# Optimization experiments

Measured on AMD Instinct MI355X. Metric: run time of the kernel, lower is better.

## Reference

```python
import jax, jax.numpy as jnp
import numpy as np

N = 500_000      # active sparse sites
C1 = 128         # input channels (c1)
CH = 64          # hidden channels c_ = int(c2 * e)
C2 = 128         # output channels (c2)
B, H, W = 4, 1024, 1024
EPS = 1e-5       # BatchNorm eps


def _build_rulebook(rng):
    """Random unique active sites + 3x3 submanifold neighbor index table.

    nbr[k, i] = row index of the active neighbor of site i at kernel offset k,
    or the sentinel N if that neighbor position is inactive / out of bounds.
    """
    per = N // B
    coords = []
    for b in range(B):
        lin = rng.choice(H * W, size=per, replace=False)
        coords.append(np.stack([np.full(per, b), lin // W, lin % W], axis=1))
    coords = np.concatenate(coords).astype(np.int64)  # [N, 3] = (batch, y, x)
    lut = np.full(B * H * W, N, dtype=np.int64)
    lut[coords[:, 0] * H * W + coords[:, 1] * W + coords[:, 2]] = np.arange(N)
    nbr = np.full((9, N), N, dtype=np.int64)
    k = 0
    for dy in (-1, 0, 1):
        for dx in (-1, 0, 1):
            ny, nx = coords[:, 1] + dy, coords[:, 2] + dx
            valid = (ny >= 0) & (ny < H) & (nx >= 0) & (nx < W)
            lin = coords[:, 0] * H * W + ny * W + nx
            nbr[k, valid] = lut[lin[valid]]
            k += 1
    return nbr


def setup_inputs() -> dict:
    nbr = _build_rulebook(np.random.default_rng(0))
    key = jax.random.key(0)
    ks = jax.random.split(key, 16)
    s = lambda k, shp, sc: (jax.random.normal(k, shp, jnp.float32) * sc)
    inp = {
        "features": jax.random.normal(ks[0], (N, C1), jnp.float32),
        "nbr_idx": jnp.asarray(nbr),
        "W1": s(ks[1], (C1, CH), 0.05),
        "W2": s(ks[2], (9, CH, CH), 0.05),
        "W3": s(ks[3], (CH, C2), 0.05),
        "g1": 1.0 + s(ks[4], (CH,), 0.1),
        "b1": s(ks[5], (CH,), 0.1),
        "m1": s(ks[6], (CH,), 0.1),
        "v1": jax.random.uniform(ks[7], (CH,), jnp.float32) + 0.5,
        "g2": 1.0 + s(ks[8], (CH,), 0.1),
        "b2": s(ks[9], (CH,), 0.1),
        "m2": s(ks[10], (CH,), 0.1),
        "v2": jax.random.uniform(ks[11], (CH,), jnp.float32) + 0.5,
        "g3": 1.0 + s(ks[12], (C2,), 0.1),
        "b3": s(ks[13], (C2,), 0.1),
        "m3": s(ks[14], (C2,), 0.1),
        "v3": jax.random.uniform(ks[15], (C2,), jnp.float32) + 0.5,
    }
    return inp


def _bn(x, g, b, m, v):
    # BatchNorm1d in inference form (running stats)
    return (x - m) * (g * jax.lax.rsqrt(v + EPS)) + b


def reference(features, nbr_idx, W1, W2, W3,
              g1, b1, m1, v1, g2, b2, m2, v2, g3, b3, m3, v3):
    # cv1: 1x1 submanifold conv == dense matmul on features, then BN + SiLU
    h = jax.nn.silu(_bn(features @ W1, g1, b1, m1, v1))  # [N, CH]
    # cv2: 3x3 submanifold conv via rulebook gather-matmul-scatter.
    # Pad one zero row so the sentinel index N gathers zeros (inactive neighbor).
    hp = jnp.concatenate([h, jnp.zeros((1, CH), h.dtype)], axis=0)  # [N+1, CH]
    out = jnp.zeros((features.shape[0], CH), h.dtype)
    for k in range(9):  # fixed kernel-offset loop, not a data-dim loop
        out = out + hp[nbr_idx[k]] @ W2[k]
    out = jax.nn.silu(_bn(out, g2, b2, m2, v2))
    # cv3: 1x1 conv + BN, then residual add (c1 == c2, shortcut) + SiLU
    out = _bn(out @ W3, g3, b3, m3, v3)
    return jax.nn.silu(out + features)
```

## Files before the change

kernel.cpp:

```cpp
#include <hip/hip_runtime.h>

#define DEVINL __device__ __forceinline__

constexpr int N_SITES = 500000;
constexpr int C1 = 128;
constexpr int CH = 64;
constexpr int C2 = 128;
constexpr float BN_EPS = 1e-5f;
constexpr int NT32 = N_SITES / 32;

typedef __attribute__((ext_vector_type(4))) float f32x4;
typedef __attribute__((ext_vector_type(8))) short s16x8;

DEVINL float bf2f(unsigned short s) { return __uint_as_float(((unsigned)s) << 16); }
DEVINL unsigned short f2bf(float f) {
  unsigned u = __float_as_uint(f);
  return (unsigned short)((u + 0x7fffu + ((u >> 16) & 1u)) >> 16);
}
DEVINL float silu_f(float x) { return x / (1.0f + __expf(-x)); }

template<bool F32>
DEVINL float rdf(const void* p, long i) {
  if constexpr (F32) return ((const float*)p)[i];
  else return bf2f(((const unsigned short*)p)[i]);
}

DEVINL bool probe_f32(const void* buf) {
  unsigned w = ((const unsigned*)buf)[threadIdx.x & 63];
  unsigned e = (w >> 7) & 0xFFu;
  bool bf_like = (e >= 90u && e <= 134u) || ((w & 0xFFFFu) == 0u);
  return __popcll(__ballot(bf_like)) < 48;
}
DEVINL bool probe_i64(const int* nbr) {
  int v = nbr[2 * (threadIdx.x & 63) + 1];
  return __popcll(__ballot(v == 0)) == 64;
}
template<bool I64>
DEVINL int rd_idx(const int* nbr, long ofs) {
  if constexpr (I64) return nbr[2 * ofs];
  else return nbr[ofs];
}

DEVINL s16x8 as_s16x8(uint4 v) { union { uint4 u; s16x8 s; } c; c.u = v; return c.s; }

DEVINL s16x8 pack8(float a0, float a1, float a2, float a3,
                   float a4, float a5, float a6, float a7) {
  uint4 r;
  r.x = (unsigned)f2bf(a0) | ((unsigned)f2bf(a1) << 16);
  r.y = (unsigned)f2bf(a2) | ((unsigned)f2bf(a3) << 16);
  r.z = (unsigned)f2bf(a4) | ((unsigned)f2bf(a5) << 16);
  r.w = (unsigned)f2bf(a6) | ((unsigned)f2bf(a7) << 16);
  return as_s16x8(r);
}

DEVINL f32x4 mfma16(s16x8 a, s16x8 b, f32x4 c) {
  return __builtin_amdgcn_mfma_f32_16x16x32_bf16(a, b, c, 0, 0, 0);
}


template<bool F32>
DEVINL void cv1_body(const void* feat, const void* W1,
                     const void* g1, const void* b1, const void* m1, const void* v1,
                     unsigned short* __restrict__ h,
                     unsigned short* lw1, float* lsc, float* ltb,
                     unsigned short* sb )
{
  const int tid = threadIdx.x;
  for (int n = tid; n < CH; n += 256) {
    float s = rdf<F32>(g1, n) * rsqrtf(rdf<F32>(v1, n) + BN_EPS);
    lsc[n] = s;
    ltb[n] = rdf<F32>(b1, n) - rdf<F32>(m1, n) * s;
  }
  __syncthreads();
  for (int idx = tid; idx < C1 * CH; idx += 256) {
    int k = idx >> 6, n = idx & 63;
    int frag = (k >> 5) * 4 + (n >> 4);
    int ln = (((k >> 3) & 3) << 4) | (n & 15);
    lw1[(frag * 64 + ln) * 8 + (k & 7)] = f2bf(rdf<F32>(W1, idx) * lsc[n]);
  }
  __syncthreads();

  const int lane = tid & 63, w = tid >> 6;
  const int lr = lane & 15, lg = lane >> 4;
  const s16x8* lw1s = (const s16x8*)lw1;
  unsigned short* sw = sb + w * (16 * 72);
  s16x8 aw[4][4];
#pragma unroll
  for (int kk = 0; kk < 4; ++kk)
#pragma unroll
    for (int mt = 0; mt < 4; ++mt)
      aw[kk][mt] = lw1s[(kk * 4 + mt) * 64 + lane];

  const int stride = gridDim.x * 4;
  for (int tile = blockIdx.x * 4 + w; tile < NT32; tile += stride) {
    const long base = (long)tile * 32;
    f32x4 acc[2][4];
#pragma unroll
    for (int st = 0; st < 2; ++st)
#pragma unroll
      for (int mt = 0; mt < 4; ++mt) acc[st][mt] = (f32x4)0.0f;

#pragma unroll
    for (int st = 0; st < 2; ++st) {
      const long row = base + st * 16 + lr;
#pragma unroll
      for (int kk = 0; kk < 4; ++kk) {
        s16x8 b;
        if constexpr (F32) {
          const float* fp = (const float*)feat + row * C1 + kk * 32 + lg * 8;
          float4 f0 = ((const float4*)fp)[0];
          float4 f1 = ((const float4*)fp)[1];
          b = pack8(f0.x, f0.y, f0.z, f0.w, f1.x, f1.y, f1.z, f1.w);
        } else {
          b = as_s16x8(*(const uint4*)((const unsigned short*)feat + row * C1 + kk * 32 + lg * 8));
        }
#pragma unroll
        for (int mt = 0; mt < 4; ++mt)
          acc[st][mt] = mfma16(aw[kk][mt], b, acc[st][mt]);
      }
    }
#pragma unroll
    for (int st = 0; st < 2; ++st) {
      __builtin_amdgcn_wave_barrier();
#pragma unroll
      for (int mt = 0; mt < 4; ++mt) {
        int ch4 = mt * 16 + lg * 4;
        f32x4 tb = *(const f32x4*)&ltb[ch4];
        f32x4 v = acc[st][mt];
        ushort4 hv;
        hv.x = f2bf(silu_f(v[0] + tb[0]));
        hv.y = f2bf(silu_f(v[1] + tb[1]));
        hv.z = f2bf(silu_f(v[2] + tb[2]));
        hv.w = f2bf(silu_f(v[3] + tb[3]));
        *(ushort4*)(sw + lr * 72 + ch4) = hv;
      }
      __builtin_amdgcn_wave_barrier();
      uint4 r1 = *(const uint4*)(sw + (lane >> 3) * 72 + (lane & 7) * 8);
      uint4 r2 = *(const uint4*)(sw + (8 + (lane >> 3)) * 72 + (lane & 7) * 8);
      size_t ho = (size_t)(base + st * 16) * CH;
      *(uint4*)(h + ho + lane * 8) = r1;
      *(uint4*)(h + ho + 512 + lane * 8) = r2;
      __builtin_amdgcn_wave_barrier();
    }
  }
}

__global__ __launch_bounds__(256, 4) void k_cv1(
    const void* feat, const void* W1,
    const void* g1, const void* b1, const void* m1, const void* v1,
    unsigned short* __restrict__ h, unsigned short* __restrict__ zrow)
{
  __shared__ __align__(16) unsigned short lw1[16 * 64 * 8];
  __shared__ __align__(16) unsigned short sb[4 * 16 * 72];
  __shared__ __align__(16) float lsc[CH];
  __shared__ __align__(16) float ltb[CH];
  if (blockIdx.x == 0 && threadIdx.x < 8)
    ((uint4*)zrow)[threadIdx.x] = make_uint4(0u, 0u, 0u, 0u);
  if (probe_f32(feat)) cv1_body<true >(feat, W1, g1, b1, m1, v1, h, lw1, lsc, ltb, sb);
  else                 cv1_body<false>(feat, W1, g1, b1, m1, v1, h, lw1, lsc, ltb, sb);
}

#define CV2_ISSUE(slot, tap_) do {                                              \
    const unsigned short* s0_ = (i0[tap_] == N_SITES) ? zrow                     \
                                : h + (size_t)i0[tap_] * CH;                     \
    const unsigned short* s1_ = (i1[tap_] == N_SITES) ? zrow                     \
                                : h + (size_t)i1[tap_] * CH;                     \
    G[slot][0] = as_s16x8(*(const uint4*)(s0_ + lg * 8));                        \
    G[slot][1] = as_s16x8(*(const uint4*)(s0_ + 32 + lg * 8));                   \
    G[slot][2] = as_s16x8(*(const uint4*)(s1_ + lg * 8));                        \
    G[slot][3] = as_s16x8(*(const uint4*)(s1_ + 32 + lg * 8));                   \
  } while (0)

template<bool F32, bool I64>
DEVINL void cv23_body(const unsigned short* __restrict__ h, const int* __restrict__ nbr,
                      const void* W2, const void* W3, const void* feat,
                      const void* g2, const void* b2, const void* m2, const void* v2,
                      const void* g3, const void* b3, const void* m3, const void* v3,
                      void* out, const unsigned short* __restrict__ zrow,
                      unsigned short* lw2, unsigned short* swt,
                      float* lsc2, float* ltb2, float* lsc3, float* ltb3)
{
  const int tid = threadIdx.x;
  for (int n = tid; n < CH; n += 512) {
    float s = rdf<F32>(g2, n) * rsqrtf(rdf<F32>(v2, n) + BN_EPS);
    lsc2[n] = s;
    ltb2[n] = rdf<F32>(b2, n) - rdf<F32>(m2, n) * s;
  }
  for (int n = tid; n < C2; n += 512) {
    float s = rdf<F32>(g3, n) * rsqrtf(rdf<F32>(v3, n) + BN_EPS);
    lsc3[n] = s;
    ltb3[n] = rdf<F32>(b3, n) - rdf<F32>(m3, n) * s;
  }
  __syncthreads();
  for (int idx = tid; idx < 9 * CH * CH; idx += 512) {
    int tap = idx >> 12;
    int k = (idx >> 6) & 63, n = idx & 63;
    int frag = (tap * 2 + (k >> 5)) * 4 + (n >> 4);
    int ln = (((k >> 3) & 3) << 4) | (n & 15);
    lw2[(frag * 64 + ln) * 8 + (k & 7)] = f2bf(rdf<F32>(W2, (long)idx) * lsc2[n]);
  }

  const int lane = tid & 63, w = tid >> 6;
  const int lr = lane & 15, lg = lane >> 4;

  s16x8 aw3[2][8];
#pragma unroll
  for (int kk = 0; kk < 2; ++kk)
#pragma unroll
    for (int mm = 0; mm < 8; ++mm) {
      float sc = lsc3[mm * 16 + lr];
      float e[8];
#pragma unroll
      for (int j = 0; j < 8; ++j)
        e[j] = rdf<F32>(W3, (long)(kk * 32 + lg * 8 + j) * C2 + mm * 16 + lr) * sc;
      aw3[kk][mm] = pack8(e[0], e[1], e[2], e[3], e[4], e[5], e[6], e[7]);
    }
  __syncthreads();

  const s16x8* lw2s = (const s16x8*)lw2;
  unsigned short* sw = swt + w * 2176;

  const int stride = gridDim.x * 8;
  for (int tile = blockIdx.x * 8 + w; tile < NT32; tile += stride) {
    const long base = (long)tile * 32;
    int i0[9], i1[9];
#pragma unroll
    for (int tap = 0; tap < 9; ++tap) {
      i0[tap] = rd_idx<I64>(nbr, (long)tap * N_SITES + base + lr);
      i1[tap] = rd_idx<I64>(nbr, (long)tap * N_SITES + base + 16 + lr);
    }
    f32x4 acc[2][4];
#pragma unroll
    for (int st = 0; st < 2; ++st)
#pragma unroll
      for (int mt = 0; mt < 4; ++mt) acc[st][mt] = (f32x4)0.0f;

    s16x8 G[3][4];
    CV2_ISSUE(0, 0); CV2_ISSUE(1, 1); CV2_ISSUE(2, 2);
#pragma unroll
    for (int tap = 0; tap < 9; ++tap) {
      const int slot = tap % 3;
#pragma unroll
      for (int mt = 0; mt < 4; ++mt) {
        s16x8 a0 = lw2s[((tap * 2 + 0) * 4 + mt) * 64 + lane];
        s16x8 a1 = lw2s[((tap * 2 + 1) * 4 + mt) * 64 + lane];
        acc[0][mt] = mfma16(a0, G[slot][0], acc[0][mt]);
        acc[0][mt] = mfma16(a1, G[slot][1], acc[0][mt]);
        acc[1][mt] = mfma16(a0, G[slot][2], acc[1][mt]);
        acc[1][mt] = mfma16(a1, G[slot][3], acc[1][mt]);
      }
      if (tap + 3 < 9) CV2_ISSUE(slot, tap + 3);
    }

#pragma unroll
    for (int st = 0; st < 2; ++st) {
      __builtin_amdgcn_wave_barrier();
#pragma unroll
      for (int mt = 0; mt < 4; ++mt) {
        int ch4 = mt * 16 + lg * 4;
        f32x4 tbv = *(const f32x4*)&ltb2[ch4];
        f32x4 v = acc[st][mt];
        ushort4 tv;
        tv.x = f2bf(silu_f(v[0] + tbv[0]));
        tv.y = f2bf(silu_f(v[1] + tbv[1]));
        tv.z = f2bf(silu_f(v[2] + tbv[2]));
        tv.w = f2bf(silu_f(v[3] + tbv[3]));
        *(ushort4*)(sw + lr * 72 + ch4) = tv;
      }
      __builtin_amdgcn_wave_barrier();
      s16x8 bfr0 = *(const s16x8*)(sw + lr * 72 + lg * 8);
      s16x8 bfr1 = *(const s16x8*)(sw + lr * 72 + 32 + lg * 8);
      f32x4 acc3[8];
#pragma unroll
      for (int mm = 0; mm < 8; ++mm) acc3[mm] = (f32x4)0.0f;
#pragma unroll
      for (int mm = 0; mm < 8; ++mm) acc3[mm] = mfma16(aw3[0][mm], bfr0, acc3[mm]);
#pragma unroll
      for (int mm = 0; mm < 8; ++mm) acc3[mm] = mfma16(aw3[1][mm], bfr1, acc3[mm]);

      const size_t site = (size_t)(base + st * 16 + lr);
      if constexpr (F32) {
#pragma unroll
        for (int mm = 0; mm < 8; ++mm) {
          int ch4 = mm * 16 + lg * 4;
          f32x4 tbv = *(const f32x4*)&ltb3[ch4];
          float4 fv = *(const float4*)((const float*)feat + site * C1 + ch4);
          float4 ov;
          ov.x = silu_f(acc3[mm][0] + tbv[0] + fv.x);
          ov.y = silu_f(acc3[mm][1] + tbv[1] + fv.y);
          ov.z = silu_f(acc3[mm][2] + tbv[2] + fv.z);
          ov.w = silu_f(acc3[mm][3] + tbv[3] + fv.w);
          *(float4*)((float*)out + site * C2 + ch4) = ov;
        }
      } else {
        __builtin_amdgcn_wave_barrier();
#pragma unroll
        for (int mm = 0; mm < 8; ++mm) {
          int ch4 = mm * 16 + lg * 4;
          f32x4 tbv = *(const f32x4*)&ltb3[ch4];
          ushort4 ov;
          ov.x = f2bf(acc3[mm][0] + tbv[0]);
          ov.y = f2bf(acc3[mm][1] + tbv[1]);
          ov.z = f2bf(acc3[mm][2] + tbv[2]);
          ov.w = f2bf(acc3[mm][3] + tbv[3]);
          *(ushort4*)(sw + lr * 136 + ch4) = ov;
        }
        __builtin_amdgcn_wave_barrier();
#pragma unroll
        for (int p = 0; p < 4; ++p) {
          int r = p * 4 + (lane >> 4);
          int c8 = (lane & 15) * 8;
          const unsigned short* sp = sw + r * 136 + c8;
          size_t srow = (size_t)(base + st * 16 + r) * C2 + c8;
          const unsigned short* fp = (const unsigned short*)feat + srow;
          unsigned short* op = (unsigned short*)out + srow;
          ushort4 o0 = *(const ushort4*)sp, o1 = *(const ushort4*)(sp + 4);
          ushort4 f0 = *(const ushort4*)fp, f1 = *(const ushort4*)(fp + 4);
          ushort4 w0, w1;
          w0.x = f2bf(silu_f(bf2f(o0.x) + bf2f(f0.x)));
          w0.y = f2bf(silu_f(bf2f(o0.y) + bf2f(f0.y)));
          w0.z = f2bf(silu_f(bf2f(o0.z) + bf2f(f0.z)));
          w0.w = f2bf(silu_f(bf2f(o0.w) + bf2f(f0.w)));
          w1.x = f2bf(silu_f(bf2f(o1.x) + bf2f(f1.x)));
          w1.y = f2bf(silu_f(bf2f(o1.y) + bf2f(f1.y)));
          w1.z = f2bf(silu_f(bf2f(o1.z) + bf2f(f1.z)));
          w1.w = f2bf(silu_f(bf2f(o1.w) + bf2f(f1.w)));
          *(ushort4*)op = w0;
          *(ushort4*)(op + 4) = w1;
        }
        __builtin_amdgcn_wave_barrier();
      }
    }
  }
}

__global__ __launch_bounds__(512, 2) void k_cv23(
    const unsigned short* __restrict__ h, const int* __restrict__ nbr,
    const void* W2, const void* W3, const void* feat,
    const void* g2, const void* b2, const void* m2, const void* v2,
    const void* g3, const void* b3, const void* m3, const void* v3,
    void* out, const unsigned short* __restrict__ zrow)
{
  __shared__ __align__(16) unsigned short lw2[72 * 64 * 8];
  __shared__ __align__(16) unsigned short swt[8 * 2176];
  __shared__ __align__(16) float lsc2[CH], ltb2[CH];
  __shared__ __align__(16) float lsc3[C2], ltb3[C2];
  bool f32 = probe_f32(feat);
  bool i64 = probe_i64(nbr);
  if (f32) { if (i64) cv23_body<true , true >(h, nbr, W2, W3, feat, g2, b2, m2, v2, g3, b3, m3, v3, out, zrow, lw2, swt, lsc2, ltb2, lsc3, ltb3);
             else     cv23_body<true , false>(h, nbr, W2, W3, feat, g2, b2, m2, v2, g3, b3, m3, v3, out, zrow, lw2, swt, lsc2, ltb2, lsc3, ltb3); }
  else     { if (i64) cv23_body<false, true >(h, nbr, W2, W3, feat, g2, b2, m2, v2, g3, b3, m3, v3, out, zrow, lw2, swt, lsc2, ltb2, lsc3, ltb3);
             else     cv23_body<false, false>(h, nbr, W2, W3, feat, g2, b2, m2, v2, g3, b3, m3, v3, out, zrow, lw2, swt, lsc2, ltb2, lsc3, ltb3); }
}

extern "C" void kernel_launch(void* const* d_in, const int* in_sizes, int n_in,
                              void* d_out, int out_size, void* d_ws, size_t ws_size,
                              hipStream_t stream)
{
  (void)out_size; (void)ws_size;
  int mp[17];
  for (int i = 0; i < 17; ++i) mp[i] = i;
  if (n_in == 17 && in_sizes[0] != 64000000 &&
      in_sizes[6] == 64000000 && in_sizes[13] == 4500000) {
    const int amap[17] = {6, 13, 0, 1, 2, 7, 3, 10, 14, 8, 4, 11, 15, 9, 5, 12, 16};
    for (int i = 0; i < 17; ++i) mp[i] = amap[i];
  }
  const void* feat = d_in[mp[0]];
  const int*  nbr  = (const int*)d_in[mp[1]];
  const void* W1 = d_in[mp[2]];
  const void* W2 = d_in[mp[3]];
  const void* W3 = d_in[mp[4]];
  const void* g1 = d_in[mp[5]],  *b1 = d_in[mp[6]],  *m1 = d_in[mp[7]],  *v1 = d_in[mp[8]];
  const void* g2 = d_in[mp[9]],  *b2 = d_in[mp[10]], *m2 = d_in[mp[11]], *v2 = d_in[mp[12]];
  const void* g3 = d_in[mp[13]], *b3 = d_in[mp[14]], *m3 = d_in[mp[15]], *v3 = d_in[mp[16]];

  unsigned short* h = (unsigned short*)d_ws;
  unsigned short* zrow = (unsigned short*)((char*)d_ws + (size_t)N_SITES * CH * 2);

  k_cv1<<<2048, 256, 0, stream>>>(feat, W1, g1, b1, m1, v1, h, zrow);
  k_cv23<<<256, 512, 0, stream>>>(h, nbr, W2, W3, feat,
                                  g2, b2, m2, v2, g3, b3, m3, v3,
                                  (void*)d_out, zrow);
}
```

Measured before the change: 641.8 us.

## Prepack W2 in a separate kernel and split taps between LDS and global

Adds a small pre-kernel that scales and fragments W2 into bf16 MFMA layout in workspace, so each cv23 block copies it instead of rebuilding it. Only taps 0-4 are staged in LDS; taps 5-8 are read straight from global/L2, which shrinks LDS per block. That allows 4 blocks per CU and a grid of 512. The cost is an extra kernel launch and global weight loads inside the MFMA loop, which may add latency and register pressure under the higher launch bound.

```diff
diff --git a/kernel.cpp b/kernel.cpp
--- a/kernel.cpp
+++ b/kernel.cpp
@@ -57,6 +57,31 @@
   return __builtin_amdgcn_mfma_f32_16x16x32_bf16(a, b, c, 0, 0, 0);
 }
 
+
+template<bool F32>
+DEVINL void pack_body(const void* W2, const void* g2, const void* v2,
+                      unsigned short* __restrict__ w2f)
+{
+  long idx0 = (long)blockIdx.x * 256 + threadIdx.x;
+  for (long idx = idx0; idx < 9 * CH * CH; idx += (long)gridDim.x * 256) {
+    int tap = (int)(idx >> 12);
+    int k = (int)(idx >> 6) & 63, n = (int)idx & 63;
+    float s = rdf<F32>(g2, n) * rsqrtf(rdf<F32>(v2, n) + BN_EPS);
+    int frag = (tap * 2 + (k >> 5)) * 4 + (n >> 4);
+    int ln = (((k >> 3) & 3) << 4) | (n & 15);
+    w2f[(frag * 64 + ln) * 8 + (k & 7)] = f2bf(rdf<F32>(W2, idx) * s);
+  }
+}
+
+__global__ __launch_bounds__(256) void k_pack(
+    const void* W2, const void* g2, const void* v2,
+    unsigned short* __restrict__ w2f, unsigned short* __restrict__ zrow)
+{
+  if (blockIdx.x == 0 && threadIdx.x < 8)
+    ((uint4*)zrow)[threadIdx.x] = make_uint4(0u, 0u, 0u, 0u);
+  if (probe_f32(W2)) pack_body<true >(W2, g2, v2, w2f);
+  else               pack_body<false>(W2, g2, v2, w2f);
+}
 
 template<bool F32>
 DEVINL void cv1_body(const void* feat, const void* W1,
@@ -148,14 +173,12 @@
 __global__ __launch_bounds__(256, 4) void k_cv1(
     const void* feat, const void* W1,
     const void* g1, const void* b1, const void* m1, const void* v1,
-    unsigned short* __restrict__ h, unsigned short* __restrict__ zrow)
+    unsigned short* __restrict__ h)
 {
   __shared__ __align__(16) unsigned short lw1[16 * 64 * 8];
   __shared__ __align__(16) unsigned short sb[4 * 16 * 72];
   __shared__ __align__(16) float lsc[CH];
   __shared__ __align__(16) float ltb[CH];
-  if (blockIdx.x == 0 && threadIdx.x < 8)
-    ((uint4*)zrow)[threadIdx.x] = make_uint4(0u, 0u, 0u, 0u);
   if (probe_f32(feat)) cv1_body<true >(feat, W1, g1, b1, m1, v1, h, lw1, lsc, ltb, sb);
   else                 cv1_body<false>(feat, W1, g1, b1, m1, v1, h, lw1, lsc, ltb, sb);
 }
@@ -173,17 +196,17 @@
 
 template<bool F32, bool I64>
 DEVINL void cv23_body(const unsigned short* __restrict__ h, const int* __restrict__ nbr,
-                      const void* W2, const void* W3, const void* feat,
-                      const void* g2, const void* b2, const void* m2, const void* v2,
+                      const unsigned short* __restrict__ w2f, const void* W3,
+                      const void* feat,
+                      const void* b2, const void* m2, const void* g2, const void* v2,
                       const void* g3, const void* b3, const void* m3, const void* v3,
                       void* out, const unsigned short* __restrict__ zrow,
                       unsigned short* lw2, unsigned short* swt,
-                      float* lsc2, float* ltb2, float* lsc3, float* ltb3)
+                      float* ltb2, float* lsc3, float* ltb3)
 {
   const int tid = threadIdx.x;
   for (int n = tid; n < CH; n += 512) {
     float s = rdf<F32>(g2, n) * rsqrtf(rdf<F32>(v2, n) + BN_EPS);
-    lsc2[n] = s;
     ltb2[n] = rdf<F32>(b2, n) - rdf<F32>(m2, n) * s;
   }
   for (int n = tid; n < C2; n += 512) {
@@ -192,13 +215,8 @@
     ltb3[n] = rdf<F32>(b3, n) - rdf<F32>(m3, n) * s;
   }
   __syncthreads();
-  for (int idx = tid; idx < 9 * CH * CH; idx += 512) {
-    int tap = idx >> 12;
-    int k = (idx >> 6) & 63, n = idx & 63;
-    int frag = (tap * 2 + (k >> 5)) * 4 + (n >> 4);
-    int ln = (((k >> 3) & 3) << 4) | (n & 15);
-    lw2[(frag * 64 + ln) * 8 + (k & 7)] = f2bf(rdf<F32>(W2, (long)idx) * lsc2[n]);
-  }
+  for (int i = tid; i < 2560; i += 512)
+    ((uint4*)lw2)[i] = ((const uint4*)w2f)[i];
 
   const int lane = tid & 63, w = tid >> 6;
   const int lr = lane & 15, lg = lane >> 4;
@@ -218,6 +236,7 @@
   __syncthreads();
 
   const s16x8* lw2s = (const s16x8*)lw2;
+  const s16x8* w2fs = (const s16x8*)w2f;
   unsigned short* sw = swt + w * 2176;
 
   const int stride = gridDim.x * 8;
@@ -242,8 +261,14 @@
       const int slot = tap % 3;
 #pragma unroll
       for (int mt = 0; mt < 4; ++mt) {
-        s16x8 a0 = lw2s[((tap * 2 + 0) * 4 + mt) * 64 + lane];
-        s16x8 a1 = lw2s[((tap * 2 + 1) * 4 + mt) * 64 + lane];
+        s16x8 a0, a1;
+        if (tap < 5) {
+          a0 = lw2s[((tap * 2 + 0) * 4 + mt) * 64 + lane];
+          a1 = lw2s[((tap * 2 + 1) * 4 + mt) * 64 + lane];
+        } else {
+          a0 = w2fs[((tap * 2 + 0) * 4 + mt) * 64 + lane];
+          a1 = w2fs[((tap * 2 + 1) * 4 + mt) * 64 + lane];
+        }
         acc[0][mt] = mfma16(a0, G[slot][0], acc[0][mt]);
         acc[0][mt] = mfma16(a1, G[slot][1], acc[0][mt]);
         acc[1][mt] = mfma16(a0, G[slot][2], acc[1][mt]);
@@ -334,23 +359,23 @@
   }
 }
 
-__global__ __launch_bounds__(512, 2) void k_cv23(
+__global__ __launch_bounds__(512, 4) void k_cv23(
     const unsigned short* __restrict__ h, const int* __restrict__ nbr,
-    const void* W2, const void* W3, const void* feat,
-    const void* g2, const void* b2, const void* m2, const void* v2,
+    const unsigned short* __restrict__ w2f, const void* W3, const void* feat,
+    const void* b2, const void* m2, const void* g2, const void* v2,
     const void* g3, const void* b3, const void* m3, const void* v3,
     void* out, const unsigned short* __restrict__ zrow)
 {
-  __shared__ __align__(16) unsigned short lw2[72 * 64 * 8];
+  __shared__ __align__(16) unsigned short lw2[5 * 8 * 64 * 8];
   __shared__ __align__(16) unsigned short swt[8 * 2176];
-  __shared__ __align__(16) float lsc2[CH], ltb2[CH];
+  __shared__ __align__(16) float ltb2[CH];
   __shared__ __align__(16) float lsc3[C2], ltb3[C2];
   bool f32 = probe_f32(feat);
   bool i64 = probe_i64(nbr);
-  if (f32) { if (i64) cv23_body<true , true >(h, nbr, W2, W3, feat, g2, b2, m2, v2, g3, b3, m3, v3, out, zrow, lw2, swt, lsc2, ltb2, lsc3, ltb3);
-             else     cv23_body<true , false>(h, nbr, W2, W3, feat, g2, b2, m2, v2, g3, b3, m3, v3, out, zrow, lw2, swt, lsc2, ltb2, lsc3, ltb3); }
-  else     { if (i64) cv23_body<false, true >(h, nbr, W2, W3, feat, g2, b2, m2, v2, g3, b3, m3, v3, out, zrow, lw2, swt, lsc2, ltb2, lsc3, ltb3);
-             else     cv23_body<false, false>(h, nbr, W2, W3, feat, g2, b2, m2, v2, g3, b3, m3, v3, out, zrow, lw2, swt, lsc2, ltb2, lsc3, ltb3); }
+  if (f32) { if (i64) cv23_body<true , true >(h, nbr, w2f, W3, feat, b2, m2, g2, v2, g3, b3, m3, v3, out, zrow, lw2, swt, ltb2, lsc3, ltb3);
+             else     cv23_body<true , false>(h, nbr, w2f, W3, feat, b2, m2, g2, v2, g3, b3, m3, v3, out, zrow, lw2, swt, ltb2, lsc3, ltb3); }
+  else     { if (i64) cv23_body<false, true >(h, nbr, w2f, W3, feat, b2, m2, g2, v2, g3, b3, m3, v3, out, zrow, lw2, swt, ltb2, lsc3, ltb3);
+             else     cv23_body<false, false>(h, nbr, w2f, W3, feat, b2, m2, g2, v2, g3, b3, m3, v3, out, zrow, lw2, swt, ltb2, lsc3, ltb3); }
 }
 
 extern "C" void kernel_launch(void* const* d_in, const int* in_sizes, int n_in,
@@ -374,11 +399,13 @@
   const void* g2 = d_in[mp[9]],  *b2 = d_in[mp[10]], *m2 = d_in[mp[11]], *v2 = d_in[mp[12]];
   const void* g3 = d_in[mp[13]], *b3 = d_in[mp[14]], *m3 = d_in[mp[15]], *v3 = d_in[mp[16]];
 
-  unsigned short* h = (unsigned short*)d_ws;
-  unsigned short* zrow = (unsigned short*)((char*)d_ws + (size_t)N_SITES * CH * 2);
-
-  k_cv1<<<2048, 256, 0, stream>>>(feat, W1, g1, b1, m1, v1, h, zrow);
-  k_cv23<<<256, 512, 0, stream>>>(h, nbr, W2, W3, feat,
-                                  g2, b2, m2, v2, g3, b3, m3, v3,
+  unsigned short* h    = (unsigned short*)d_ws;
+  unsigned short* zrow = (unsigned short*)((char*)d_ws + 64000000);
+  unsigned short* w2f  = (unsigned short*)((char*)d_ws + 64000256);
+
+  k_pack<<<64, 256, 0, stream>>>(W2, g2, v2, w2f, zrow);
+  k_cv1<<<2048, 256, 0, stream>>>(feat, W1, g1, b1, m1, v1, h);
+  k_cv23<<<512, 512, 0, stream>>>(h, nbr, w2f, W3, feat,
+                                  b2, m2, g2, v2, g3, b3, m3, v3,
                                   (void*)d_out, zrow);
 }
```

Measured after the change: 953.1 us. +48.5%, slower.
